# Kernel tuning notes

Measured on AMD Instinct MI355X. Metric: run time of the kernel, lower is better.

The kernel has to match this reference:

```python
import jax, jax.numpy as jnp
import numpy as np

K = 3          # s_kernel_size = max_graph_distance + 1
C_OUT = 128    # out_channel


def setup_inputs() -> dict:
    key = jax.random.key(0)
    k1, k2, k3, k4 = jax.random.split(key, 4)
    N, C_IN, T, V = 64, 64, 256, 25
    x = jax.random.normal(k1, (N, C_IN, T, V), dtype=jnp.float32)
    # 1x1 Conv2d(in_channel, out_channel*K) weight/bias
    W = jax.random.normal(k2, (K * C_OUT, C_IN), dtype=jnp.float32) * 0.05
    b = jax.random.normal(k3, (K * C_OUT,), dtype=jnp.float32) * 0.05
    # fixed adjacency stack (non-trainable buffer-like param)
    A = jax.random.uniform(k4, (K, V, V), dtype=jnp.float32)
    edge = jnp.ones((K, V, V), dtype=jnp.float32)       # init ones_like(A)
    adaptive_A = jnp.zeros((K, V, V), dtype=jnp.float32)  # init zeros_like(A)
    return {"x": x, "W": W, "b": b, "A": A, "edge": edge, "adaptive_A": adaptive_A}


def reference(x, W, b, A, edge, adaptive_A):
    n, c_in, t, v = x.shape
    # 1x1 conv == per-pixel GEMM over channel dim: (n,c,t,v) -> (n, K*C_OUT, t, v)
    y = jnp.einsum('nctv,oc->notv', x, W) + b[None, :, None, None]
    y = y.reshape(n, K, C_OUT, t, v)                 # (n, k, c, t, v)
    effective_A = A * edge + adaptive_A              # (k, v, w)
    out = jnp.einsum('nkctv,kvw->nctw', y, effective_A)
    return out
```

## Files before the change

### kernel.cpp

```cpp
#include <hip/hip_runtime.h>
#include <hip/hip_bf16.h>

typedef __bf16 bf16x8 __attribute__((ext_vector_type(8)));
typedef __bf16 bf16x4 __attribute__((ext_vector_type(4)));
typedef float floatx4 __attribute__((ext_vector_type(4)));
typedef float floatx4u __attribute__((ext_vector_type(4), aligned(4)));

#define ROWK 200
#define ZROWS 100

__global__ void sgc_prep(const float* __restrict__ W, const float* __restrict__ b,
                         const float* __restrict__ A, const float* __restrict__ edge,
                         const float* __restrict__ adA,
                         __hip_bfloat16* __restrict__ Wp, __hip_bfloat16* __restrict__ effAB,
                         float* __restrict__ bias2T) {
  int tid = blockIdx.x * blockDim.x + threadIdx.x;
  int nthr = gridDim.x * blockDim.x;
  for (int i = tid; i < 24576; i += nthr) {
    int c = i / 192; int r = i - c * 192; int k = r >> 6; int ci = r & 63;
    Wp[i] = __float2bfloat16(W[(k * 128 + c) * 64 + ci]);
  }
  for (int i = tid; i < 2560; i += nthr) {
    int n = i >> 5; int v = i & 31;
    float val = 0.f;
    if (n < 75 && v < 25) {
      int k = n / 25; int w = n - k * 25;
      int idx = (k * 25 + v) * 25 + w;
      val = A[idx] * edge[idx] + adA[idx];
    }
    effAB[i] = __float2bfloat16(val);
  }
  for (int i = tid; i < 3200; i += nthr) {
    int w = i >> 7; int c = i & 127;
    float s = 0.f;
    for (int k = 0; k < 3; k++) {
      float sv = 0.f;
      for (int v = 0; v < 25; v++) {
        int idx = (k * 25 + v) * 25 + w;
        sv += A[idx] * edge[idx] + adA[idx];
      }
      s += b[k * 128 + c] * sv;
    }
    bias2T[i] = s;
  }
}

__global__ __launch_bounds__(256, 3)
void sgc_main(const float* __restrict__ x,
              const __hip_bfloat16* __restrict__ Wp,
              const __hip_bfloat16* __restrict__ effAB,
              const float* __restrict__ bias2T,
              float* __restrict__ out) {
  __shared__ __hip_bfloat16 lds[ZROWS * ROWK];
  __hip_bfloat16* zt = lds;
  float* xs = (float*)lds;
  float* eb = (float*)lds;

  const int tid = threadIdx.x;
  const int lane = tid & 63;
  const int wv = tid >> 6;
  const int blk0 = blockIdx.x;
  const int blk = (blk0 & 7) * 512 + (blk0 >> 3);
  const int col = lane & 15;
  const int quad = lane >> 4;
  const int kb = quad * 8;
  const int g0 = blk * 4;
  const int n = g0 >> 8, t0 = g0 & 255;

  floatx4 xr[7];
  const float* xn = x + (size_t)n * 64 * 6400 + t0 * 25;
#pragma unroll
  for (int i = 0; i < 7; i++) {
    int f = tid + 256 * i;
    if (f < 1600) {
      int ci = f / 25, q = f - ci * 25;
      xr[i] = *(const floatx4u*)(xn + (size_t)ci * 6400 + q * 4);
    }
  }

  bf16x8 afr[2][6];
#pragma unroll
  for (int mtl = 0; mtl < 2; mtl++) {
    int c = (2 * wv + mtl) * 16 + col;
    const __hip_bfloat16* wrow = Wp + c * 192;
#pragma unroll
    for (int ks = 0; ks < 6; ks++)
      afr[mtl][ks] = *(const bf16x8*)(wrow + ks * 32 + kb);
  }

  bf16x8 bA[5];
#pragma unroll
  for (int nt = 0; nt < 5; nt++)
    bA[nt] = *(const bf16x8*)(effAB + (nt * 16 + col) * 32 + kb);

#pragma unroll
  for (int i = 0; i < 7; i++) {
    int f = tid + 256 * i;
    if (f < 1600) {
      int ci = f / 25;
      int q4 = (f - ci * 25) * 4;
#pragma unroll
      for (int e = 0; e < 4; e++) {
        int rr = q4 + e;
        int tt = rr / 25, v = rr - tt * 25;
        xs[(tt * 64 + ci) * 28 + v] = xr[i][e];
      }
    }
  }

  floatx4 acc[2][7];
#pragma unroll
  for (int nt = 0; nt < 7; nt++) {
    int nn = nt * 16 + col;
    int p = (nn * 41) >> 10;
    int w = nn - p * 25;
#pragma unroll
    for (int mtl = 0; mtl < 2; mtl++) {
      int c0 = (2 * wv + mtl) * 16 + quad * 4;
      acc[mtl][nt] = *(const floatx4*)(bias2T + w * 128 + c0);
    }
  }

  __syncthreads();

  bf16x8 xa[4];
#pragma unroll
  for (int mt = 0; mt < 4; mt++) {
    int ci = mt * 16 + col;
    const float* base = xs + (wv * 64 + ci) * 28;
    if (quad < 3) {
      floatx4 a = *(const floatx4*)(base + kb);
      floatx4 c = *(const floatx4*)(base + kb + 4);
      xa[mt] = (bf16x8){(__bf16)a.x, (__bf16)a.y, (__bf16)a.z, (__bf16)a.w,
                        (__bf16)c.x, (__bf16)c.y, (__bf16)c.z, (__bf16)c.w};
    } else {
      float v24 = base[24];
      xa[mt] = (bf16x8){(__bf16)v24, (__bf16)0.f, (__bf16)0.f, (__bf16)0.f,
                        (__bf16)0.f, (__bf16)0.f, (__bf16)0.f, (__bf16)0.f};
    }
  }

  __syncthreads();

#pragma unroll
  for (int mt = 0; mt < 4; mt++) {
    floatx4 zacc[5];
#pragma unroll
    for (int nt = 0; nt < 5; nt++) {
      zacc[nt] = (floatx4){0.f, 0.f, 0.f, 0.f};
      zacc[nt] = __builtin_amdgcn_mfma_f32_16x16x32_bf16(xa[mt], bA[nt], zacc[nt], 0, 0, 0);
    }
#pragma unroll
    for (int nt = 0; nt < 5; nt++) {
      int nn = nt * 16 + col;
      if (nn < 75) {
        int k = (nn * 41) >> 10;
        int w = nn - k * 25;
        bf16x4 zb = (bf16x4){(__bf16)zacc[nt][0], (__bf16)zacc[nt][1],
                             (__bf16)zacc[nt][2], (__bf16)zacc[nt][3]};
        *(bf16x4*)(zt + (wv * 25 + w) * ROWK + k * 64 + mt * 16 + quad * 4) = zb;
      }
    }
  }

  int zoff[7];
#pragma unroll
  for (int nt = 0; nt < 7; nt++) {
    int nn = nt * 16 + col;
    int rr = (nt == 6) ? (nn < 100 ? nn : 99) : nn;
    zoff[nt] = rr * ROWK + kb;
  }

  __syncthreads();

#pragma unroll
  for (int ks = 0; ks < 6; ks++) {
    bf16x8 bfr[7];
#pragma unroll
    for (int nt = 0; nt < 7; nt++)
      bfr[nt] = *(const bf16x8*)(zt + zoff[nt] + ks * 32);
#pragma unroll
    for (int nt = 0; nt < 7; nt++) {
      acc[0][nt] = __builtin_amdgcn_mfma_f32_16x16x32_bf16(afr[0][ks], bfr[nt], acc[0][nt], 0, 0, 0);
      acc[1][nt] = __builtin_amdgcn_mfma_f32_16x16x32_bf16(afr[1][ks], bfr[nt], acc[1][nt], 0, 0, 0);
    }
  }

  __syncthreads();

#pragma unroll
  for (int h = 0; h < 2; h++) {
    int slotbase = wv * 16 + quad * 4;
#pragma unroll
    for (int nt = 0; nt < 7; nt++) {
      int nn = nt * 16 + col;
      if (nn < 100) {
#pragma unroll
        for (int r = 0; r < 4; r++)
          eb[(slotbase + r) * 100 + nn] = acc[h][nt][r];
      }
    }
    __syncthreads();
#pragma unroll
    for (int i = 0; i < 7; i++) {
      int f = tid + 256 * i;
      if (f < 1600) {
        int slot = f / 25, q = f - slot * 25;
        floatx4 v = *(const floatx4*)(eb + slot * 100 + q * 4);
        int c = 32 * (slot >> 4) + 16 * h + (slot & 15);
        float* ob = out + ((size_t)(n * 128 + c) * 256 + t0) * 25 + q * 4;
        *(floatx4u*)ob = v;
      }
    }
    __syncthreads();
  }
}

extern "C" void kernel_launch(void* const* d_in, const int* in_sizes, int n_in,
                              void* d_out, int out_size, void* d_ws, size_t ws_size,
                              hipStream_t stream) {
  const float* x    = (const float*)d_in[0];
  const float* W    = (const float*)d_in[1];
  const float* b    = (const float*)d_in[2];
  const float* A    = (const float*)d_in[3];
  const float* edge = (const float*)d_in[4];
  const float* adA  = (const float*)d_in[5];
  float* out = (float*)d_out;

  char* ws = (char*)d_ws;
  __hip_bfloat16* Wp    = (__hip_bfloat16*)ws;
  __hip_bfloat16* effAB = (__hip_bfloat16*)(ws + 49152);
  float* bias2T         = (float*)(ws + 54272);

  sgc_prep<<<64, 256, 0, stream>>>(W, b, A, edge, adA, Wp, effAB, bias2T);
  sgc_main<<<4096, 256, 0, stream>>>(x, Wp, effAB, bias2T, out);
}
```

Before: 363.4 us.

## Split second GEMM into two column phases to raise occupancy to 4 blocks

Splits the W-by-Z MFMA stage into two passes over output column tiles (4 then 3), so fewer accumulators are live at once. Loading of the W fragments is moved later to shorten their live range. Launch bounds go from 3 to 4 blocks per SM to trade registers for more resident waves. The epilogue is reordered so the first half of phase A is written to LDS while phase B computes, at the cost of the W-fragment loads now sitting on the critical path after the LDS barrier.

```diff
diff --git a/kernel.cpp b/kernel.cpp
--- a/kernel.cpp
+++ b/kernel.cpp
@@ -45,7 +45,7 @@
   }
 }
 
-__global__ __launch_bounds__(256, 3)
+__global__ __launch_bounds__(256, 4)
 void sgc_main(const float* __restrict__ x,
               const __hip_bfloat16* __restrict__ Wp,
               const __hip_bfloat16* __restrict__ effAB,
@@ -78,20 +78,23 @@
     }
   }
 
-  bf16x8 afr[2][6];
-#pragma unroll
-  for (int mtl = 0; mtl < 2; mtl++) {
-    int c = (2 * wv + mtl) * 16 + col;
-    const __hip_bfloat16* wrow = Wp + c * 192;
-#pragma unroll
-    for (int ks = 0; ks < 6; ks++)
-      afr[mtl][ks] = *(const bf16x8*)(wrow + ks * 32 + kb);
-  }
-
   bf16x8 bA[5];
 #pragma unroll
   for (int nt = 0; nt < 5; nt++)
     bA[nt] = *(const bf16x8*)(effAB + (nt * 16 + col) * 32 + kb);
+
+  floatx4 accA[2][4];
+#pragma unroll
+  for (int nt = 0; nt < 4; nt++) {
+    int nn = nt * 16 + col;
+    int p = (nn * 41) >> 10;
+    int w = nn - p * 25;
+#pragma unroll
+    for (int mtl = 0; mtl < 2; mtl++) {
+      int c0 = (2 * wv + mtl) * 16 + quad * 4;
+      accA[mtl][nt] = *(const floatx4*)(bias2T + w * 128 + c0);
+    }
+  }
 
 #pragma unroll
   for (int i = 0; i < 7; i++) {
@@ -105,19 +108,6 @@
         int tt = rr / 25, v = rr - tt * 25;
         xs[(tt * 64 + ci) * 28 + v] = xr[i][e];
       }
-    }
-  }
-
-  floatx4 acc[2][7];
-#pragma unroll
-  for (int nt = 0; nt < 7; nt++) {
-    int nn = nt * 16 + col;
-    int p = (nn * 41) >> 10;
-    int w = nn - p * 25;
-#pragma unroll
-    for (int mtl = 0; mtl < 2; mtl++) {
-      int c0 = (2 * wv + mtl) * 16 + quad * 4;
-      acc[mtl][nt] = *(const floatx4*)(bias2T + w * 128 + c0);
     }
   }
 
@@ -163,56 +153,138 @@
     }
   }
 
-  int zoff[7];
-#pragma unroll
-  for (int nt = 0; nt < 7; nt++) {
-    int nn = nt * 16 + col;
-    int rr = (nt == 6) ? (nn < 100 ? nn : 99) : nn;
-    zoff[nt] = rr * ROWK + kb;
+  bf16x8 afr[2][6];
+#pragma unroll
+  for (int mtl = 0; mtl < 2; mtl++) {
+    int c = (2 * wv + mtl) * 16 + col;
+    const __hip_bfloat16* wrow = Wp + c * 192;
+#pragma unroll
+    for (int ks = 0; ks < 6; ks++)
+      afr[mtl][ks] = *(const bf16x8*)(wrow + ks * 32 + kb);
   }
 
   __syncthreads();
 
 #pragma unroll
   for (int ks = 0; ks < 6; ks++) {
-    bf16x8 bfr[7];
-#pragma unroll
-    for (int nt = 0; nt < 7; nt++)
-      bfr[nt] = *(const bf16x8*)(zt + zoff[nt] + ks * 32);
-#pragma unroll
-    for (int nt = 0; nt < 7; nt++) {
-      acc[0][nt] = __builtin_amdgcn_mfma_f32_16x16x32_bf16(afr[0][ks], bfr[nt], acc[0][nt], 0, 0, 0);
-      acc[1][nt] = __builtin_amdgcn_mfma_f32_16x16x32_bf16(afr[1][ks], bfr[nt], acc[1][nt], 0, 0, 0);
-    }
-  }
-
-  __syncthreads();
-
-#pragma unroll
-  for (int h = 0; h < 2; h++) {
+    bf16x8 bfr[4];
+#pragma unroll
+    for (int nt = 0; nt < 4; nt++)
+      bfr[nt] = *(const bf16x8*)(zt + (nt * 16 + col) * ROWK + ks * 32 + kb);
+#pragma unroll
+    for (int nt = 0; nt < 4; nt++) {
+      accA[0][nt] = __builtin_amdgcn_mfma_f32_16x16x32_bf16(afr[0][ks], bfr[nt], accA[0][nt], 0, 0, 0);
+      accA[1][nt] = __builtin_amdgcn_mfma_f32_16x16x32_bf16(afr[1][ks], bfr[nt], accA[1][nt], 0, 0, 0);
+    }
+  }
+
+  __syncthreads();
+
+  {
     int slotbase = wv * 16 + quad * 4;
 #pragma unroll
-    for (int nt = 0; nt < 7; nt++) {
+    for (int nt = 0; nt < 4; nt++) {
       int nn = nt * 16 + col;
+#pragma unroll
+      for (int r = 0; r < 4; r++)
+        eb[(slotbase + r) * 100 + nn] = accA[0][nt][r];
+    }
+  }
+
+  floatx4 accB[2][3];
+#pragma unroll
+  for (int nt = 0; nt < 3; nt++) {
+    int nn = (nt + 4) * 16 + col;
+    int p = (nn * 41) >> 10;
+    int w = nn - p * 25;
+#pragma unroll
+    for (int mtl = 0; mtl < 2; mtl++) {
+      int c0 = (2 * wv + mtl) * 16 + quad * 4;
+      accB[mtl][nt] = *(const floatx4*)(bias2T + w * 128 + c0);
+    }
+  }
+
+  int zoffB[3];
+#pragma unroll
+  for (int nt = 0; nt < 3; nt++) {
+    int nn = (nt + 4) * 16 + col;
+    int rr = (nt == 2) ? (nn < 100 ? nn : 99) : nn;
+    zoffB[nt] = rr * ROWK + kb;
+  }
+#pragma unroll
+  for (int ks = 0; ks < 6; ks++) {
+    bf16x8 bfr[3];
+#pragma unroll
+    for (int nt = 0; nt < 3; nt++)
+      bfr[nt] = *(const bf16x8*)(zt + zoffB[nt] + ks * 32);
+#pragma unroll
+    for (int nt = 0; nt < 3; nt++) {
+      accB[0][nt] = __builtin_amdgcn_mfma_f32_16x16x32_bf16(afr[0][ks], bfr[nt], accB[0][nt], 0, 0, 0);
+      accB[1][nt] = __builtin_amdgcn_mfma_f32_16x16x32_bf16(afr[1][ks], bfr[nt], accB[1][nt], 0, 0, 0);
+    }
+  }
+
+  {
+    int slotbase = wv * 16 + quad * 4;
+#pragma unroll
+    for (int nt = 0; nt < 3; nt++) {
+      int nn = (nt + 4) * 16 + col;
       if (nn < 100) {
 #pragma unroll
         for (int r = 0; r < 4; r++)
-          eb[(slotbase + r) * 100 + nn] = acc[h][nt][r];
-      }
-    }
-    __syncthreads();
-#pragma unroll
-    for (int i = 0; i < 7; i++) {
-      int f = tid + 256 * i;
-      if (f < 1600) {
-        int slot = f / 25, q = f - slot * 25;
-        floatx4 v = *(const floatx4*)(eb + slot * 100 + q * 4);
-        int c = 32 * (slot >> 4) + 16 * h + (slot & 15);
-        float* ob = out + ((size_t)(n * 128 + c) * 256 + t0) * 25 + q * 4;
-        *(floatx4u*)ob = v;
-      }
-    }
-    __syncthreads();
+          eb[(slotbase + r) * 100 + nn] = accB[0][nt][r];
+      }
+    }
+  }
+
+  __syncthreads();
+
+#pragma unroll
+  for (int i = 0; i < 7; i++) {
+    int f = tid + 256 * i;
+    if (f < 1600) {
+      int slot = f / 25, q = f - slot * 25;
+      floatx4 v = *(const floatx4*)(eb + slot * 100 + q * 4);
+      int c = 32 * (slot >> 4) + (slot & 15);
+      float* ob = out + ((size_t)(n * 128 + c) * 256 + t0) * 25 + q * 4;
+      *(floatx4u*)ob = v;
+    }
+  }
+
+  __syncthreads();
+
+  {
+    int slotbase = wv * 16 + quad * 4;
+#pragma unroll
+    for (int nt = 0; nt < 4; nt++) {
+      int nn = nt * 16 + col;
+#pragma unroll
+      for (int r = 0; r < 4; r++)
+        eb[(slotbase + r) * 100 + nn] = accA[1][nt][r];
+    }
+#pragma unroll
+    for (int nt = 0; nt < 3; nt++) {
+      int nn = (nt + 4) * 16 + col;
+      if (nn < 100) {
+#pragma unroll
+        for (int r = 0; r < 4; r++)
+          eb[(slotbase + r) * 100 + nn] = accB[1][nt][r];
+      }
+    }
+  }
+
+  __syncthreads();
+
+#pragma unroll
+  for (int i = 0; i < 7; i++) {
+    int f = tid + 256 * i;
+    if (f < 1600) {
+      int slot = f / 25, q = f - slot * 25;
+      floatx4 v = *(const floatx4*)(eb + slot * 100 + q * 4);
+      int c = 32 * (slot >> 4) + 16 + (slot & 15);
+      float* ob = out + ((size_t)(n * 128 + c) * 256 + t0) * 25 + q * 4;
+      *(floatx4u*)ob = v;
+    }
   }
 }
 
```

Result: faster. 346.5 us, median of 2 (-4.6%).
